# Kernel optimization log

Hardware: AMD Instinct MI355X
Metric: run time of the kernel (lower is better)

The kernel has to match this reference:

```python
import jax, jax.numpy as jnp
import numpy as np

E = 8          # num_experts
TOP_K = 2
D = 512        # embed_dim
H = 1024       # expert_dim = 2 * embed_dim
B, S = 16, 4096


def setup_inputs() -> dict:
    key = jax.random.key(0)
    ks = jax.random.split(key, 10)
    sd = lambda fan_in: 1.0 / np.sqrt(fan_in)
    x = jax.random.normal(ks[0], (B, S, D), dtype=jnp.float32)
    # gate: Linear(D, D//2) -> ReLU -> Linear(D//2, E)
    gw1 = jax.random.uniform(ks[1], (D, D // 2), jnp.float32, -sd(D), sd(D))
    gb1 = jnp.zeros((D // 2,), jnp.float32)
    gw2 = jax.random.uniform(ks[2], (D // 2, E), jnp.float32, -sd(D // 2), sd(D // 2))
    gb2 = jnp.zeros((E,), jnp.float32)
    # stacked experts: Linear(D, H) -> GELU -> Linear(H, D)  (dropout inactive / eval)
    we1 = jax.random.uniform(ks[3], (E, D, H), jnp.float32, -sd(D), sd(D))
    be1 = jnp.zeros((E, H), jnp.float32)
    we2 = jax.random.uniform(ks[4], (E, H, D), jnp.float32, -sd(H), sd(H))
    be2 = jnp.zeros((E, D), jnp.float32)
    return {"x": x, "gw1": gw1, "gb1": gb1, "gw2": gw2, "gb2": gb2,
            "we1": we1, "be1": be1, "we2": we2, "be2": be2}


def reference(x, gw1, gb1, gw2, gb2, we1, be1, we2, be2):
    b, s, d = x.shape
    xf = x.reshape(-1, d)                              # [T, D]
    T = xf.shape[0]

    # Gating network: softmax over experts
    gate_logits = jax.nn.relu(xf @ gw1 + gb1) @ gw2 + gb2   # [T, E]
    gate_weights = jax.nn.softmax(gate_logits, axis=-1)

    # Top-k selection, then re-softmax over the selected probabilities
    # (matches torch: softmax applied to the top-k *probabilities*)
    top_w, top_idx = jax.lax.top_k(gate_weights, TOP_K)    # [T, K]
    top_w = jax.nn.softmax(top_w, axis=-1)

    # Combine weights per (token, expert): zero where expert not selected
    combine = jnp.zeros((T, E), dtype=xf.dtype)
    combine = combine.at[jnp.arange(T)[:, None], top_idx].add(top_w)  # [T, E]

    # Expert MLPs (dropout in eval mode is identity); weight-by-combine is
    # mathematically identical to the masked dispatch in the original.
    out = jnp.zeros_like(xf)
    for e in range(E):
        h = jax.nn.gelu(xf @ we1[e] + be1[e], approximate=False)  # [T, H]
        y = h @ we2[e] + be2[e]                                   # [T, D]
        out = out + combine[:, e:e + 1] * y

    return out.reshape(b, s, d)
```

## Files before the change

### kernel.cpp

```cpp
#include <hip/hip_runtime.h>
#include <hip/hip_bf16.h>
#include <math.h>


typedef __attribute__((ext_vector_type(8))) short bf16x8;
typedef __attribute__((ext_vector_type(4))) float f32x4;

__device__ __forceinline__ unsigned short f2bf(float f){
  unsigned u = __builtin_bit_cast(unsigned, f);
  u += 0x7FFFu + ((u >> 16) & 1u);
  return (unsigned short)(u >> 16);
}

__device__ __forceinline__ bf16x8 cvt8(float4 f0, float4 f1){
  bf16x8 r;
  r[0]=(short)f2bf(f0.x); r[1]=(short)f2bf(f0.y); r[2]=(short)f2bf(f0.z); r[3]=(short)f2bf(f0.w);
  r[4]=(short)f2bf(f1.x); r[5]=(short)f2bf(f1.y); r[6]=(short)f2bf(f1.z); r[7]=(short)f2bf(f1.w);
  return r;
}

__device__ __forceinline__ void gload16(const void* g, void* l){
  __builtin_amdgcn_global_load_lds((const __attribute__((address_space(1))) unsigned int*)g,
                                   (__attribute__((address_space(3))) unsigned int*)l, 16, 0, 0);
}

__global__ __launch_bounds__(256)
void xcvt_kernel(const float* __restrict__ x, unsigned short* __restrict__ xbf){
  int i = blockIdx.x * 256 + threadIdx.x;
  const float4 f0 = ((const float4*)x)[(size_t)i * 2];
  const float4 f1 = ((const float4*)x)[(size_t)i * 2 + 1];
  ushort4 o0, o1;
  o0.x = f2bf(f0.x); o0.y = f2bf(f0.y); o0.z = f2bf(f0.z); o0.w = f2bf(f0.w);
  o1.x = f2bf(f1.x); o1.y = f2bf(f1.y); o1.z = f2bf(f1.z); o1.w = f2bf(f1.w);
  ((ushort4*)xbf)[(size_t)i * 2]     = o0;
  ((ushort4*)xbf)[(size_t)i * 2 + 1] = o1;
}

__global__ __launch_bounds__(256, 4)
void transpose_cvt_kernel(const float* __restrict__ in, unsigned short* __restrict__ out,
                          int R, int C){
  const int tilesR = R >> 6, tilesC = C >> 6;
  const int b = blockIdx.x;
  const int e = b / (tilesR * tilesC);
  const int rem = b % (tilesR * tilesC);
  const int rb = (rem / tilesC) << 6;
  const int cb = (rem % tilesC) << 6;
  const float* src = in + (size_t)e * R * C;
  unsigned short* dst = out + (size_t)e * R * C;
  __shared__ float t[64][65];
  const int r0 = threadIdx.x >> 4;
  const int c4 = (threadIdx.x & 15) << 2;
  #pragma unroll
  for (int p = 0; p < 4; ++p){
    int r = r0 + (p << 4);
    const float4 v = *(const float4*)(src + (size_t)(rb + r) * C + cb + c4);
    t[r][c4+0] = v.x; t[r][c4+1] = v.y; t[r][c4+2] = v.z; t[r][c4+3] = v.w;
  }
  __syncthreads();
  #pragma unroll
  for (int p = 0; p < 4; ++p){
    int cr = r0 + (p << 4);
    ushort4 o;
    o.x = f2bf(t[c4+0][cr]); o.y = f2bf(t[c4+1][cr]);
    o.z = f2bf(t[c4+2][cr]); o.w = f2bf(t[c4+3][cr]);
    *(ushort4*)(dst + (size_t)(cb + cr) * R + rb + c4) = o;
  }
}

__global__ __launch_bounds__(512, 4)
void gate_gemm1_kernel(const float* __restrict__ x, const float* __restrict__ gw1,
                       const float* __restrict__ gb1, float* __restrict__ h){
  __shared__ float xs[32][68];
  __shared__ float g1s[32][256];
  const int tid = threadIdx.x;
  const int t0 = blockIdx.x << 6;
  const int tg = tid >> 6;
  const int cg = tid & 63;

  const int xtok = tid >> 3, xk4 = (tid & 7) << 2;
  const int gr = tid >> 6, gc = (tid & 63) << 2;

  float acc0[4] = {0.f,0.f,0.f,0.f}, acc1[4] = {0.f,0.f,0.f,0.f};
  float acc2[4] = {0.f,0.f,0.f,0.f}, acc3[4] = {0.f,0.f,0.f,0.f};
  float acc4[4] = {0.f,0.f,0.f,0.f}, acc5[4] = {0.f,0.f,0.f,0.f};
  float acc6[4] = {0.f,0.f,0.f,0.f}, acc7[4] = {0.f,0.f,0.f,0.f};

  for (int kb = 0; kb < 512; kb += 32){
    __syncthreads();
    {
      const float4 v = *(const float4*)(x + (size_t)(t0 + xtok) * 512 + kb + xk4);
      xs[xk4+0][xtok] = v.x; xs[xk4+1][xtok] = v.y;
      xs[xk4+2][xtok] = v.z; xs[xk4+3][xtok] = v.w;
    }
    #pragma unroll
    for (int p = 0; p < 4; ++p)
      *(float4*)&g1s[(p << 3) + gr][gc] =
        *(const float4*)(gw1 + (size_t)(kb + (p << 3) + gr) * 256 + gc);
    __syncthreads();
    #pragma unroll 4
    for (int k = 0; k < 32; ++k){
      const float4 wv = *(const float4*)&g1s[k][cg << 2];
      const float4 xa = *(const float4*)&xs[k][tg << 3];
      const float4 xb = *(const float4*)&xs[k][(tg << 3) + 4];
      acc0[0]=fmaf(xa.x,wv.x,acc0[0]); acc0[1]=fmaf(xa.x,wv.y,acc0[1]);
      acc0[2]=fmaf(xa.x,wv.z,acc0[2]); acc0[3]=fmaf(xa.x,wv.w,acc0[3]);
      acc1[0]=fmaf(xa.y,wv.x,acc1[0]); acc1[1]=fmaf(xa.y,wv.y,acc1[1]);
      acc1[2]=fmaf(xa.y,wv.z,acc1[2]); acc1[3]=fmaf(xa.y,wv.w,acc1[3]);
      acc2[0]=fmaf(xa.z,wv.x,acc2[0]); acc2[1]=fmaf(xa.z,wv.y,acc2[1]);
      acc2[2]=fmaf(xa.z,wv.z,acc2[2]); acc2[3]=fmaf(xa.z,wv.w,acc2[3]);
      acc3[0]=fmaf(xa.w,wv.x,acc3[0]); acc3[1]=fmaf(xa.w,wv.y,acc3[1]);
      acc3[2]=fmaf(xa.w,wv.z,acc3[2]); acc3[3]=fmaf(xa.w,wv.w,acc3[3]);
      acc4[0]=fmaf(xb.x,wv.x,acc4[0]); acc4[1]=fmaf(xb.x,wv.y,acc4[1]);
      acc4[2]=fmaf(xb.x,wv.z,acc4[2]); acc4[3]=fmaf(xb.x,wv.w,acc4[3]);
      acc5[0]=fmaf(xb.y,wv.x,acc5[0]); acc5[1]=fmaf(xb.y,wv.y,acc5[1]);
      acc5[2]=fmaf(xb.y,wv.z,acc5[2]); acc5[3]=fmaf(xb.y,wv.w,acc5[3]);
      acc6[0]=fmaf(xb.z,wv.x,acc6[0]); acc6[1]=fmaf(xb.z,wv.y,acc6[1]);
      acc6[2]=fmaf(xb.z,wv.z,acc6[2]); acc6[3]=fmaf(xb.z,wv.w,acc6[3]);
      acc7[0]=fmaf(xb.w,wv.x,acc7[0]); acc7[1]=fmaf(xb.w,wv.y,acc7[1]);
      acc7[2]=fmaf(xb.w,wv.z,acc7[2]); acc7[3]=fmaf(xb.w,wv.w,acc7[3]);
    }
  }

  const float4 bias = *(const float4*)(gb1 + (cg << 2));
  float* hp = h + (size_t)(t0 + (tg << 3)) * 256 + (cg << 2);
  float4 o;
  #define HOUT(ACC, T) \
    o.x = fmaxf(ACC[0] + bias.x, 0.f); o.y = fmaxf(ACC[1] + bias.y, 0.f); \
    o.z = fmaxf(ACC[2] + bias.z, 0.f); o.w = fmaxf(ACC[3] + bias.w, 0.f); \
    *(float4*)(hp + (size_t)(T) * 256) = o;
  HOUT(acc0, 0) HOUT(acc1, 1) HOUT(acc2, 2) HOUT(acc3, 3)
  HOUT(acc4, 4) HOUT(acc5, 5) HOUT(acc6, 6) HOUT(acc7, 7)
  #undef HOUT
}

__global__ __launch_bounds__(256, 2)
void gate2_kernel(const float* __restrict__ h, const float* __restrict__ gw2,
                  const float* __restrict__ gb2,
                  int* __restrict__ counts, int* __restrict__ pair_tok,
                  float* __restrict__ pair_w){
  __shared__ float g2s[256 * 9];
  __shared__ int   lcnt[8];
  __shared__ int   lbase[8];
  __shared__ int   lpre[9];
  __shared__ int   ltok[8][256];
  __shared__ float lw[8][256];
  const int tid = threadIdx.x;
  const int t0 = blockIdx.x << 8;

  #pragma unroll
  for (int p = 0; p < 8; ++p){
    int idx = tid + (p << 8);
    g2s[(idx >> 3) * 9 + (idx & 7)] = gw2[idx];
  }
  if (tid < 8) lcnt[tid] = 0;
  __syncthreads();

  const int token = t0 + tid;
  float pl[8];
  #pragma unroll
  for (int e = 0; e < 8; ++e) pl[e] = gb2[e];
  for (int j = 0; j < 64; ++j){
    const float4 hv = *(const float4*)(h + (size_t)token * 256 + (j << 2));
    #pragma unroll
    for (int i = 0; i < 4; ++i){
      const float hx = ((const float*)&hv)[i];
      #pragma unroll
      for (int e = 0; e < 8; ++e)
        pl[e] = fmaf(hx, g2s[((j << 2) + i) * 9 + e], pl[e]);
    }
  }
  float m = pl[0];
  #pragma unroll
  for (int e = 1; e < 8; ++e) m = fmaxf(m, pl[e]);
  float p[8]; float s = 0.f;
  #pragma unroll
  for (int e = 0; e < 8; ++e){ p[e] = expf(pl[e] - m); s += p[e]; }
  float inv = 1.f / s;
  float m1 = -1.f, m2 = -1.f; int i1 = 0, i2 = 0;
  #pragma unroll
  for (int e = 0; e < 8; ++e){
    float pe = p[e] * inv;
    if (pe > m1){ m2 = m1; i2 = i1; m1 = pe; i1 = e; }
    else if (pe > m2){ m2 = pe; i2 = e; }
  }
  float e21 = expf(m2 - m1);
  float w1 = 1.f / (1.f + e21);
  float w2 = 1.f - w1;
  int p1 = atomicAdd(&lcnt[i1], 1); ltok[i1][p1] = token; lw[i1][p1] = w1;
  int p2 = atomicAdd(&lcnt[i2], 1); ltok[i2][p2] = token; lw[i2][p2] = w2;
  __syncthreads();
  if (tid < 8) lbase[tid] = atomicAdd(&counts[tid], lcnt[tid]);
  if (tid == 0){
    lpre[0] = 0;
    #pragma unroll
    for (int e = 0; e < 8; ++e) lpre[e+1] = lpre[e] + lcnt[e];
  }
  __syncthreads();
  const int total = lpre[8];
  for (int idx = tid; idx < total; idx += 256){
    int e = 0;
    #pragma unroll
    for (int q = 0; q < 7; ++q) e += (idx >= lpre[q + 1]) ? 1 : 0;
    const int i = idx - lpre[e];
    const int dst = (e << 16) + lbase[e] + i;
    pair_tok[dst] = ltok[e][i];
    pair_w[dst]   = lw[e][i];
  }
}

__global__ void scan_kernel(const int* __restrict__ counts, int* __restrict__ offs,
                            int* __restrict__ toffs){
  if (threadIdx.x == 0){
    int o = 0, t = 0;
    #pragma unroll
    for (int e = 0; e < 8; ++e){
      offs[e] = o; o += (counts[e] + 127) >> 7;
      toffs[e] = t; t += counts[e];
    }
    offs[8] = o; toffs[8] = t;
  }
}

__global__ __launch_bounds__(256, 4)
void eg1_kernel(const unsigned short* __restrict__ xbf,
                const unsigned short* __restrict__ we1T,
                const float* __restrict__ be1,
                const int* __restrict__ counts, const int* __restrict__ offs,
                const int* __restrict__ toffs, const int* __restrict__ pair_tok,
                unsigned short* __restrict__ h){
  const int g = (blockIdx.x & 7) * 1032 + (blockIdx.x >> 3);
  const int chunk = g >> 3, nt = g & 7;
  if (chunk >= offs[8]) return;
  int e = 0;
  #pragma unroll
  for (int q = 0; q < 7; ++q) e += (chunk >= offs[q+1]) ? 1 : 0;
  const int cnt = counts[e];
  const int base = (chunk - offs[e]) << 7;
  const int n0 = nt << 7;
  const int tid = threadIdx.x;
  const int lane = tid & 63;
  const int wv = tid >> 6;
  const int wr = wv >> 1, wc = wv & 1;
  const int lrow = lane & 15, kgrp = lane >> 4;

  __shared__ char lds[32768];
  char* const As = lds;
  char* const Bs = lds + 16384;

  const int srow = tid >> 3;
  const int sdelta = ((tid & 7) << 4) ^ ((srow & 7) << 4);
  unsigned aoff[4];
  #pragma unroll
  for (int i = 0; i < 4; ++i){
    int rr = base + srow + (i << 5);
    int tok = (rr < cnt) ? pair_tok[(e << 16) + rr] : 0;
    aoff[i] = ((unsigned)tok) << 10;
  }
  const char* const xb  = (const char*)xbf;
  const char* const w1b = (const char*)we1T + ((size_t)e << 20);

  f32x4 acc[4][4];
  #pragma unroll
  for (int i = 0; i < 4; ++i)
    #pragma unroll
    for (int j = 0; j < 4; ++j) acc[i][j] = (f32x4)0.f;

  const int sw = (lrow & 7) << 4;
  for (int kb = 0; kb < 8; ++kb){
    #pragma unroll
    for (int i = 0; i < 4; ++i)
      gload16(xb + aoff[i] + (kb << 7) + sdelta, As + (tid << 4) + (i << 12));
    #pragma unroll
    for (int i = 0; i < 4; ++i)
      gload16(w1b + (size_t)(n0 + srow + (i << 5)) * 1024 + (kb << 7) + sdelta,
              Bs + (tid << 4) + (i << 12));
    __syncthreads();
    #pragma unroll
    for (int s = 0; s < 2; ++s){
      const int kbyte = ((s << 6) + (kgrp << 4)) ^ sw;
      bf16x8 af[4], bf[4];
      #pragma unroll
      for (int f = 0; f < 4; ++f){
        af[f] = *(const bf16x8*)(As + ((wr << 6) + (f << 4) + lrow) * 128 + kbyte);
        bf[f] = *(const bf16x8*)(Bs + ((wc << 6) + (f << 4) + lrow) * 128 + kbyte);
      }
      #pragma unroll
      for (int fb = 0; fb < 4; ++fb)
        #pragma unroll
        for (int fa = 0; fa < 4; ++fa)
          acc[fb][fa] = __builtin_amdgcn_mfma_f32_16x16x32_bf16(bf[fb], af[fa], acc[fb][fa], 0, 0, 0);
    }
    __syncthreads();
  }

  const int hrow0 = toffs[e] + base;
  float4 bias4[4];
  #pragma unroll
  for (int fb = 0; fb < 4; ++fb)
    bias4[fb] = *(const float4*)(be1 + (e << 10) + n0 + (wc << 6) + (fb << 4) + (kgrp << 2));
  #pragma unroll
  for (int fa = 0; fa < 4; ++fa){
    const int tl = (wr << 6) + (fa << 4) + lrow;
    if (base + tl < cnt){
      unsigned short* hp = h + (size_t)(hrow0 + tl) * 1024 + n0 + (wc << 6) + (kgrp << 2);
      #pragma unroll
      for (int fb = 0; fb < 4; ++fb){
        float v, gl; ushort4 o;
        v = acc[fb][fa][0] + bias4[fb].x; gl = 0.5f*v*(1.f+erff(v*0.70710678118654752f)); o.x = f2bf(gl);
        v = acc[fb][fa][1] + bias4[fb].y; gl = 0.5f*v*(1.f+erff(v*0.70710678118654752f)); o.y = f2bf(gl);
        v = acc[fb][fa][2] + bias4[fb].z; gl = 0.5f*v*(1.f+erff(v*0.70710678118654752f)); o.z = f2bf(gl);
        v = acc[fb][fa][3] + bias4[fb].w; gl = 0.5f*v*(1.f+erff(v*0.70710678118654752f)); o.w = f2bf(gl);
        *(ushort4*)(hp + (fb << 4)) = o;
      }
    }
  }
}

__global__ __launch_bounds__(256, 4)
void eg2_kernel(const unsigned short* __restrict__ h,
                const unsigned short* __restrict__ we2T,
                const float* __restrict__ be2,
                const int* __restrict__ counts, const int* __restrict__ offs,
                const int* __restrict__ toffs, const int* __restrict__ pair_tok,
                const float* __restrict__ pair_w,
                float* __restrict__ out){
  const int g = (blockIdx.x & 7) * 516 + (blockIdx.x >> 3);
  const int chunk = g >> 2, nt = g & 3;
  if (chunk >= offs[8]) return;
  int e = 0;
  #pragma unroll
  for (int q = 0; q < 7; ++q) e += (chunk >= offs[q+1]) ? 1 : 0;
  const int cnt = counts[e];
  const int base = (chunk - offs[e]) << 7;
  const int n0 = nt << 7;
  const int tid = threadIdx.x;
  const int lane = tid & 63;
  const int wv = tid >> 6;
  const int wr = wv >> 1, wc = wv & 1;
  const int lrow = lane & 15, kgrp = lane >> 4;

  __shared__ char lds[32768];
  char* const As = lds;
  char* const Bs = lds + 16384;

  const int srow = tid >> 3;
  const int sdelta = ((tid & 7) << 4) ^ ((srow & 7) << 4);
  const char* const hb  = (const char*)h + (size_t)(toffs[e] + base) * 2048;
  const char* const w2b = (const char*)we2T + ((size_t)e << 20);

  f32x4 acc[4][4];
  #pragma unroll
  for (int i = 0; i < 4; ++i)
    #pragma unroll
    for (int j = 0; j < 4; ++j) acc[i][j] = (f32x4)0.f;

  const int sw = (lrow & 7) << 4;
  for (int kb = 0; kb < 16; ++kb){
    #pragma unroll
    for (int i = 0; i < 4; ++i)
      gload16(hb + (size_t)(srow + (i << 5)) * 2048 + (kb << 7) + sdelta,
              As + (tid << 4) + (i << 12));
    #pragma unroll
    for (int i = 0; i < 4; ++i)
      gload16(w2b + (size_t)(n0 + srow + (i << 5)) * 2048 + (kb << 7) + sdelta,
              Bs + (tid << 4) + (i << 12));
    __syncthreads();
    #pragma unroll
    for (int s = 0; s < 2; ++s){
      const int kbyte = ((s << 6) + (kgrp << 4)) ^ sw;
      bf16x8 af[4], bf[4];
      #pragma unroll
      for (int f = 0; f < 4; ++f){
        af[f] = *(const bf16x8*)(As + ((wr << 6) + (f << 4) + lrow) * 128 + kbyte);
        bf[f] = *(const bf16x8*)(Bs + ((wc << 6) + (f << 4) + lrow) * 128 + kbyte);
      }
      #pragma unroll
      for (int fr = 0; fr < 4; ++fr)
        #pragma unroll
        for (int fc = 0; fc < 4; ++fc)
          acc[fr][fc] = __builtin_amdgcn_mfma_f32_16x16x32_bf16(af[fr], bf[fc], acc[fr][fc], 0, 0, 0);
    }
    __syncthreads();
  }

  float bias2[4];
  #pragma unroll
  for (int fc = 0; fc < 4; ++fc)
    bias2[fc] = be2[(e << 9) + n0 + (wc << 6) + (fc << 4) + lrow];

  #pragma unroll
  for (int fr = 0; fr < 4; ++fr){
    #pragma unroll
    for (int rg = 0; rg < 4; ++rg){
      const int rloc = (wr << 6) + (fr << 4) + (kgrp << 2) + rg;
      const int r = base + rloc;
      if (r < cnt){
        const int tok = pair_tok[(e << 16) + r];
        const float wgt = pair_w[(e << 16) + r];
        float* const orow = out + (size_t)tok * 512 + n0 + (wc << 6) + lrow;
        #pragma unroll
        for (int fc = 0; fc < 4; ++fc)
          atomicAdd(orow + (fc << 4), wgt * (acc[fr][fc][rg] + bias2[fc]));
      }
    }
  }
}

#define VW2() asm volatile("s_waitcnt vmcnt(2)" ::: "memory")
#define BAR() __builtin_amdgcn_s_barrier()
#define SB0() __builtin_amdgcn_sched_barrier(0)

#define G1_MFMA(S, BUF) do{ \
  __builtin_amdgcn_s_setprio(1); \
  _Pragma("unroll") \
  for (int ct = 0; ct < 4; ++ct){ \
    const int col = (ct << 4) + lrow; \
    const int swc = (col & 7) << 4; \
    _Pragma("unroll") \
    for (int k2 = 0; k2 < 4; ++k2){ \
      const int byt = (col << 8) + ((((k2) << 6) + (kgrp << 4)) ^ swc); \
      bf16x8 bfr = *(const bf16x8*)((const char*)(BUF) + byt); \
      hacc[ct] = __builtin_amdgcn_mfma_f32_16x16x32_bf16(a[(S)*4 + k2], bfr, hacc[ct], 0, 0, 0); \
    } \
  } \
  __builtin_amdgcn_s_setprio(0); \
}while(0)

#define G2_MFMA(NB, BUF) do{ \
  __builtin_amdgcn_s_setprio(1); \
  _Pragma("unroll") \
  for (int nt2 = 0; nt2 < 8; ++nt2){ \
    const int col = (nt2 << 4) + lrow; \
    const int swc = (col & 7) << 4; \
    _Pragma("unroll") \
    for (int k2 = 0; k2 < 2; ++k2){ \
      const int byt = (col << 7) + (((k2 << 6) + (kgrp << 4)) ^ swc); \
      bf16x8 bfr = *(const bf16x8*)((const char*)(BUF) + byt); \
      acc[(NB)*8 + nt2] = __builtin_amdgcn_mfma_f32_16x16x32_bf16(a2[k2], bfr, acc[(NB)*8 + nt2], 0, 0, 0); \
    } \
  } \
  __builtin_amdgcn_s_setprio(0); \
}while(0)

#define PHASE(STAGE_STMT, MFMA_STMT) do{ \
  STAGE_STMT; VW2(); BAR(); SB0(); MFMA_STMT; SB0(); BAR(); }while(0)

__global__ __launch_bounds__(512, 2)
void expert_kernel(const unsigned short* __restrict__ xbf,
                   const unsigned short* __restrict__ we1T,
                   const unsigned short* __restrict__ we2T,
                   const float* __restrict__ be1, const float* __restrict__ be2,
                   const int* __restrict__ counts, const int* __restrict__ offs,
                   const int* __restrict__ pair_tok, const float* __restrict__ pair_w,
                   float* __restrict__ out){
  const int b = blockIdx.x;
  if (b >= offs[8]) return;
  int e = 0;
  #pragma unroll
  for (int q = 0; q < 7; ++q) e += (b >= offs[q + 1]) ? 1 : 0;
  const int cnt = counts[e];
  const int base = (b - offs[e]) << 7;
  const int tid = threadIdx.x;
  const int wv = tid >> 6;
  const int lane = tid & 63;
  const int lrow = lane & 15;
  const int kgrp = lane >> 4;

  __shared__ unsigned short w1s0[64 * 128];
  __shared__ unsigned short w1s1[64 * 128];
  __shared__ unsigned short w2s0[128 * 64];
  __shared__ unsigned short w2s1[128 * 64];
  __shared__ unsigned short hs[128 * 64];

  bf16x8 a[16];
  {
    int r = base + (wv << 4) + lrow;
    int tok = (r < cnt) ? pair_tok[(e << 16) + r] : 0;
    const unsigned short* xr = xbf + (size_t)tok * 512 + (kgrp << 3);
    #pragma unroll
    for (int kc = 0; kc < 16; ++kc)
      a[kc] = *(const bf16x8*)(xr + (kc << 5));
  }
  f32x4 acc[32];
  #pragma unroll
  for (int i = 0; i < 32; ++i) acc[i] = (f32x4)0.f;

  const unsigned short* w1g = we1T + ((size_t)e << 19);
  const unsigned short* w2g = we2T + ((size_t)e << 19);

  auto stage_w1 = [&](int hcv, int s, unsigned short* buf){
    #pragma unroll
    for (int i = 0; i < 2; ++i){
      int bb = (((wv << 1) + i) << 10) + (lane << 4);
      int row = bb >> 8;
      int inner = bb & 255;
      int srcb = ((hcv + row) << 10) + (s << 8) + (inner ^ ((row & 7) << 4));
      gload16((const char*)w1g + srcb, (char*)buf + (((wv << 1) + i) << 10));
    }
  };
  auto stage_w2 = [&](int hcv, int nb, unsigned short* buf){
    #pragma unroll
    for (int i = 0; i < 2; ++i){
      int bb = (((wv << 1) + i) << 10) + (lane << 4);
      int row = bb >> 7;
      int inner = bb & 127;
      int srcb = (((nb << 7) + row) << 11) + (hcv << 1) + (inner ^ ((row & 7) << 4));
      gload16((const char*)w2g + srcb, (char*)buf + (((wv << 1) + i) << 10));
    }
  };

  stage_w1(0, 0, w1s0);

  for (int hc = 0; hc < 1024; hc += 64){
    f32x4 hacc[4];
    #pragma unroll
    for (int i = 0; i < 4; ++i) hacc[i] = (f32x4)0.f;

    PHASE(stage_w1(hc, 1, w1s1), G1_MFMA(0, w1s0));
    PHASE(stage_w1(hc, 2, w1s0), G1_MFMA(1, w1s1));
    PHASE(stage_w1(hc, 3, w1s1), G1_MFMA(2, w1s0));
    PHASE(stage_w2(hc, 0, w2s0), G1_MFMA(3, w1s1));

    bf16x8 a2[2];
    {
      char* const hsb = (char*)hs;
      #pragma unroll
      for (int ct = 0; ct < 4; ++ct){
        int colL = (ct << 4) + lrow;
        float bias = be1[(e << 10) + hc + colL];
        #pragma unroll
        for (int rr = 0; rr < 4; ++rr){
          int rowL = (wv << 4) + (kgrp << 2) + rr;
          float v = hacc[ct][rr] + bias;
          float g = 0.5f * v * (1.f + erff(v * 0.70710678118654752f));
          int byt = (rowL << 7) + (colL << 1);
          *(unsigned short*)(hsb + (byt ^ ((rowL & 7) << 4))) = f2bf(g);
        }
      }
      const char* const hsc = (const char*)hs;
      int rowL = (wv << 4) + lrow;
      int swr = (rowL & 7) << 4;
      #pragma unroll
      for (int k2 = 0; k2 < 2; ++k2){
        int byt = (rowL << 7) + (((k2 << 6) + (kgrp << 4)) ^ swr);
        a2[k2] = *(const bf16x8*)(hsc + byt);
      }
    }

    PHASE(stage_w2(hc, 1, w2s1),               G2_MFMA(0, w2s0));
    PHASE(stage_w2(hc, 2, w2s0),               G2_MFMA(1, w2s1));
    PHASE(stage_w2(hc, 3, w2s1),               G2_MFMA(2, w2s0));
    PHASE(stage_w1((hc + 64) & 1023, 0, w1s0), G2_MFMA(3, w2s1));
  }

  #pragma unroll
  for (int rr = 0; rr < 4; ++rr){
    int rowL = (wv << 4) + (kgrp << 2) + rr;
    int rg = base + rowL;
    if (rg < cnt){
      int tok = pair_tok[(e << 16) + rg];
      float wp = pair_w[(e << 16) + rg];
      float* orow = out + (size_t)tok * 512;
      #pragma unroll
      for (int tl = 0; tl < 32; ++tl){
        int col = (tl << 4) + lrow;
        atomicAdd(orow + col, wp * (acc[tl][rr] + be2[(e << 9) + col]));
      }
    }
  }
}

extern "C" void kernel_launch(void* const* d_in, const int* in_sizes, int n_in,
                              void* d_out, int out_size, void* d_ws, size_t ws_size,
                              hipStream_t stream){
  const float* x   = (const float*)d_in[0];
  const float* gw1 = (const float*)d_in[1];
  const float* gb1 = (const float*)d_in[2];
  const float* gw2 = (const float*)d_in[3];
  const float* gb2 = (const float*)d_in[4];
  const float* we1 = (const float*)d_in[5];
  const float* be1 = (const float*)d_in[6];
  const float* we2 = (const float*)d_in[7];
  const float* be2 = (const float*)d_in[8];
  float* out = (float*)d_out;

  char* ws = (char*)d_ws;
  const size_t MiB = 1024 * 1024;
  unsigned short* we1T = (unsigned short*)(ws);
  unsigned short* we2T = (unsigned short*)(ws + 8 * MiB);
  int*   pair_tok = (int*)  (ws + 16 * MiB);
  float* pair_w   = (float*)(ws + 18 * MiB);
  int*   counts   = (int*)  (ws + 20 * MiB);
  int*   offs     = (int*)  (ws + 20 * MiB + 256);
  int*   toffs    = (int*)  (ws + 20 * MiB + 512);
  unsigned short* xbf  = (unsigned short*)(ws + 21 * MiB);
  float* ghuf          = (float*)(ws + 85 * MiB);
  unsigned short* hexp = (unsigned short*)(ws + 85 * MiB);
  const bool big = ws_size >= 344 * MiB;

  hipMemsetAsync(d_out, 0, (size_t)out_size * sizeof(float), stream);
  hipMemsetAsync(counts, 0, 256, stream);

  hipLaunchKernelGGL(xcvt_kernel, dim3(16384), dim3(256), 0, stream, x, xbf);
  hipLaunchKernelGGL(transpose_cvt_kernel, dim3(1024), dim3(256), 0, stream,
                     we1, we1T, 512, 1024);
  hipLaunchKernelGGL(transpose_cvt_kernel, dim3(1024), dim3(256), 0, stream,
                     we2, we2T, 1024, 512);
  hipLaunchKernelGGL(gate_gemm1_kernel, dim3(1024), dim3(512), 0, stream,
                     x, gw1, gb1, ghuf);
  hipLaunchKernelGGL(gate2_kernel, dim3(256), dim3(256), 0, stream,
                     ghuf, gw2, gb2, counts, pair_tok, pair_w);
  hipLaunchKernelGGL(scan_kernel, dim3(1), dim3(64), 0, stream, counts, offs, toffs);

  if (big){
    hipLaunchKernelGGL(eg1_kernel, dim3(8256), dim3(256), 0, stream,
                       xbf, we1T, be1, counts, offs, toffs, pair_tok, hexp);
    hipLaunchKernelGGL(eg2_kernel, dim3(4128), dim3(256), 0, stream,
                       hexp, we2T, be2, counts, offs, toffs, pair_tok, pair_w, out);
  } else {
    hipLaunchKernelGGL(expert_kernel, dim3(1032), dim3(512), 0, stream,
                       xbf, we1T, we2T, be1, be2, counts, offs, pair_tok, pair_w, out);
  }
}
```

Before: 799.6 us.

## Double-buffer LDS in expert GEMMs, fuse x conversion into gate GEMM, drop fused path

Result: slower. 895.1 us (+11.9%).

```diff
diff --git a/kernel.cpp b/kernel.cpp
--- a/kernel.cpp
+++ b/kernel.cpp
@@ -12,28 +12,9 @@
   return (unsigned short)(u >> 16);
 }
 
-__device__ __forceinline__ bf16x8 cvt8(float4 f0, float4 f1){
-  bf16x8 r;
-  r[0]=(short)f2bf(f0.x); r[1]=(short)f2bf(f0.y); r[2]=(short)f2bf(f0.z); r[3]=(short)f2bf(f0.w);
-  r[4]=(short)f2bf(f1.x); r[5]=(short)f2bf(f1.y); r[6]=(short)f2bf(f1.z); r[7]=(short)f2bf(f1.w);
-  return r;
-}
-
 __device__ __forceinline__ void gload16(const void* g, void* l){
   __builtin_amdgcn_global_load_lds((const __attribute__((address_space(1))) unsigned int*)g,
                                    (__attribute__((address_space(3))) unsigned int*)l, 16, 0, 0);
-}
-
-__global__ __launch_bounds__(256)
-void xcvt_kernel(const float* __restrict__ x, unsigned short* __restrict__ xbf){
-  int i = blockIdx.x * 256 + threadIdx.x;
-  const float4 f0 = ((const float4*)x)[(size_t)i * 2];
-  const float4 f1 = ((const float4*)x)[(size_t)i * 2 + 1];
-  ushort4 o0, o1;
-  o0.x = f2bf(f0.x); o0.y = f2bf(f0.y); o0.z = f2bf(f0.z); o0.w = f2bf(f0.w);
-  o1.x = f2bf(f1.x); o1.y = f2bf(f1.y); o1.z = f2bf(f1.z); o1.w = f2bf(f1.w);
-  ((ushort4*)xbf)[(size_t)i * 2]     = o0;
-  ((ushort4*)xbf)[(size_t)i * 2 + 1] = o1;
 }
 
 __global__ __launch_bounds__(256, 4)
@@ -69,7 +50,8 @@
 
 __global__ __launch_bounds__(512, 4)
 void gate_gemm1_kernel(const float* __restrict__ x, const float* __restrict__ gw1,
-                       const float* __restrict__ gb1, float* __restrict__ h){
+                       const float* __restrict__ gb1, float* __restrict__ h,
+                       unsigned short* __restrict__ xbf){
   __shared__ float xs[32][68];
   __shared__ float g1s[32][256];
   const int tid = threadIdx.x;
@@ -91,6 +73,9 @@
       const float4 v = *(const float4*)(x + (size_t)(t0 + xtok) * 512 + kb + xk4);
       xs[xk4+0][xtok] = v.x; xs[xk4+1][xtok] = v.y;
       xs[xk4+2][xtok] = v.z; xs[xk4+3][xtok] = v.w;
+      ushort4 o;
+      o.x = f2bf(v.x); o.y = f2bf(v.y); o.z = f2bf(v.z); o.w = f2bf(v.w);
+      *(ushort4*)(xbf + (size_t)(t0 + xtok) * 512 + kb + xk4) = o;
     }
     #pragma unroll
     for (int p = 0; p < 4; ++p)
@@ -221,7 +206,7 @@
   }
 }
 
-__global__ __launch_bounds__(256, 4)
+__global__ __launch_bounds__(256, 2)
 void eg1_kernel(const unsigned short* __restrict__ xbf,
                 const unsigned short* __restrict__ we1T,
                 const float* __restrict__ be1,
@@ -243,9 +228,7 @@
   const int wr = wv >> 1, wc = wv & 1;
   const int lrow = lane & 15, kgrp = lane >> 4;
 
-  __shared__ char lds[32768];
-  char* const As = lds;
-  char* const Bs = lds + 16384;
+  __shared__ char lds[65536];
 
   const int srow = tid >> 3;
   const int sdelta = ((tid & 7) << 4) ^ ((srow & 7) << 4);
@@ -265,16 +248,24 @@
     #pragma unroll
     for (int j = 0; j < 4; ++j) acc[i][j] = (f32x4)0.f;
 
-  const int sw = (lrow & 7) << 4;
-  for (int kb = 0; kb < 8; ++kb){
+  auto stage = [&](int kb, char* dbase){
     #pragma unroll
     for (int i = 0; i < 4; ++i)
-      gload16(xb + aoff[i] + (kb << 7) + sdelta, As + (tid << 4) + (i << 12));
+      gload16(xb + aoff[i] + (kb << 7) + sdelta, dbase + (tid << 4) + (i << 12));
     #pragma unroll
     for (int i = 0; i < 4; ++i)
       gload16(w1b + (size_t)(n0 + srow + (i << 5)) * 1024 + (kb << 7) + sdelta,
-              Bs + (tid << 4) + (i << 12));
-    __syncthreads();
+              dbase + 16384 + (tid << 4) + (i << 12));
+  };
+
+  const int sw = (lrow & 7) << 4;
+  stage(0, lds);
+  __syncthreads();
+  int cur = 0;
+  for (int kb = 0; kb < 8; ++kb){
+    if (kb < 7) stage(kb + 1, lds + ((cur ^ 1) << 15));
+    const char* const As = lds + (cur << 15);
+    const char* const Bs = As + 16384;
     #pragma unroll
     for (int s = 0; s < 2; ++s){
       const int kbyte = ((s << 6) + (kgrp << 4)) ^ sw;
@@ -290,7 +281,11 @@
         for (int fa = 0; fa < 4; ++fa)
           acc[fb][fa] = __builtin_amdgcn_mfma_f32_16x16x32_bf16(bf[fb], af[fa], acc[fb][fa], 0, 0, 0);
     }
-    __syncthreads();
+    if (kb < 7){
+      asm volatile("s_waitcnt vmcnt(0)" ::: "memory");
+      __builtin_amdgcn_s_barrier();
+    }
+    cur ^= 1;
   }
 
   const int hrow0 = toffs[e] + base;
@@ -316,7 +311,7 @@
   }
 }
 
-__global__ __launch_bounds__(256, 4)
+__global__ __launch_bounds__(256, 2)
 void eg2_kernel(const unsigned short* __restrict__ h,
                 const unsigned short* __restrict__ we2T,
                 const float* __restrict__ be2,
@@ -339,9 +334,7 @@
   const int wr = wv >> 1, wc = wv & 1;
   const int lrow = lane & 15, kgrp = lane >> 4;
 
-  __shared__ char lds[32768];
-  char* const As = lds;
-  char* const Bs = lds + 16384;
+  __shared__ char lds[65536];
 
   const int srow = tid >> 3;
   const int sdelta = ((tid & 7) << 4) ^ ((srow & 7) << 4);
@@ -354,17 +347,25 @@
     #pragma unroll
     for (int j = 0; j < 4; ++j) acc[i][j] = (f32x4)0.f;
 
-  const int sw = (lrow & 7) << 4;
-  for (int kb = 0; kb < 16; ++kb){
+  auto stage = [&](int kb, char* dbase){
     #pragma unroll
     for (int i = 0; i < 4; ++i)
       gload16(hb + (size_t)(srow + (i << 5)) * 2048 + (kb << 7) + sdelta,
-              As + (tid << 4) + (i << 12));
+              dbase + (tid << 4) + (i << 12));
     #pragma unroll
     for (int i = 0; i < 4; ++i)
       gload16(w2b + (size_t)(n0 + srow + (i << 5)) * 2048 + (kb << 7) + sdelta,
-              Bs + (tid << 4) + (i << 12));
-    __syncthreads();
+              dbase + 16384 + (tid << 4) + (i << 12));
+  };
+
+  const int sw = (lrow & 7) << 4;
+  stage(0, lds);
+  __syncthreads();
+  int cur = 0;
+  for (int kb = 0; kb < 16; ++kb){
+    if (kb < 15) stage(kb + 1, lds + ((cur ^ 1) << 15));
+    const char* const As = lds + (cur << 15);
+    const char* const Bs = As + 16384;
     #pragma unroll
     for (int s = 0; s < 2; ++s){
       const int kbyte = ((s << 6) + (kgrp << 4)) ^ sw;
@@ -380,7 +381,11 @@
         for (int fc = 0; fc < 4; ++fc)
           acc[fr][fc] = __builtin_amdgcn_mfma_f32_16x16x32_bf16(af[fr], bf[fc], acc[fr][fc], 0, 0, 0);
     }
-    __syncthreads();
+    if (kb < 15){
+      asm volatile("s_waitcnt vmcnt(0)" ::: "memory");
+      __builtin_amdgcn_s_barrier();
+    }
+    cur ^= 1;
   }
 
   float bias2[4];
@@ -401,170 +406,6 @@
         #pragma unroll
         for (int fc = 0; fc < 4; ++fc)
           atomicAdd(orow + (fc << 4), wgt * (acc[fr][fc][rg] + bias2[fc]));
-      }
-    }
-  }
-}
-
-#define VW2() asm volatile("s_waitcnt vmcnt(2)" ::: "memory")
-#define BAR() __builtin_amdgcn_s_barrier()
-#define SB0() __builtin_amdgcn_sched_barrier(0)
-
-#define G1_MFMA(S, BUF) do{ \
-  __builtin_amdgcn_s_setprio(1); \
-  _Pragma("unroll") \
-  for (int ct = 0; ct < 4; ++ct){ \
-    const int col = (ct << 4) + lrow; \
-    const int swc = (col & 7) << 4; \
-    _Pragma("unroll") \
-    for (int k2 = 0; k2 < 4; ++k2){ \
-      const int byt = (col << 8) + ((((k2) << 6) + (kgrp << 4)) ^ swc); \
-      bf16x8 bfr = *(const bf16x8*)((const char*)(BUF) + byt); \
-      hacc[ct] = __builtin_amdgcn_mfma_f32_16x16x32_bf16(a[(S)*4 + k2], bfr, hacc[ct], 0, 0, 0); \
-    } \
-  } \
-  __builtin_amdgcn_s_setprio(0); \
-}while(0)
-
-#define G2_MFMA(NB, BUF) do{ \
-  __builtin_amdgcn_s_setprio(1); \
-  _Pragma("unroll") \
-  for (int nt2 = 0; nt2 < 8; ++nt2){ \
-    const int col = (nt2 << 4) + lrow; \
-    const int swc = (col & 7) << 4; \
-    _Pragma("unroll") \
-    for (int k2 = 0; k2 < 2; ++k2){ \
-      const int byt = (col << 7) + (((k2 << 6) + (kgrp << 4)) ^ swc); \
-      bf16x8 bfr = *(const bf16x8*)((const char*)(BUF) + byt); \
-      acc[(NB)*8 + nt2] = __builtin_amdgcn_mfma_f32_16x16x32_bf16(a2[k2], bfr, acc[(NB)*8 + nt2], 0, 0, 0); \
-    } \
-  } \
-  __builtin_amdgcn_s_setprio(0); \
-}while(0)
-
-#define PHASE(STAGE_STMT, MFMA_STMT) do{ \
-  STAGE_STMT; VW2(); BAR(); SB0(); MFMA_STMT; SB0(); BAR(); }while(0)
-
-__global__ __launch_bounds__(512, 2)
-void expert_kernel(const unsigned short* __restrict__ xbf,
-                   const unsigned short* __restrict__ we1T,
-                   const unsigned short* __restrict__ we2T,
-                   const float* __restrict__ be1, const float* __restrict__ be2,
-                   const int* __restrict__ counts, const int* __restrict__ offs,
-                   const int* __restrict__ pair_tok, const float* __restrict__ pair_w,
-                   float* __restrict__ out){
-  const int b = blockIdx.x;
-  if (b >= offs[8]) return;
-  int e = 0;
-  #pragma unroll
-  for (int q = 0; q < 7; ++q) e += (b >= offs[q + 1]) ? 1 : 0;
-  const int cnt = counts[e];
-  const int base = (b - offs[e]) << 7;
-  const int tid = threadIdx.x;
-  const int wv = tid >> 6;
-  const int lane = tid & 63;
-  const int lrow = lane & 15;
-  const int kgrp = lane >> 4;
-
-  __shared__ unsigned short w1s0[64 * 128];
-  __shared__ unsigned short w1s1[64 * 128];
-  __shared__ unsigned short w2s0[128 * 64];
-  __shared__ unsigned short w2s1[128 * 64];
-  __shared__ unsigned short hs[128 * 64];
-
-  bf16x8 a[16];
-  {
-    int r = base + (wv << 4) + lrow;
-    int tok = (r < cnt) ? pair_tok[(e << 16) + r] : 0;
-    const unsigned short* xr = xbf + (size_t)tok * 512 + (kgrp << 3);
-    #pragma unroll
-    for (int kc = 0; kc < 16; ++kc)
-      a[kc] = *(const bf16x8*)(xr + (kc << 5));
-  }
-  f32x4 acc[32];
-  #pragma unroll
-  for (int i = 0; i < 32; ++i) acc[i] = (f32x4)0.f;
-
-  const unsigned short* w1g = we1T + ((size_t)e << 19);
-  const unsigned short* w2g = we2T + ((size_t)e << 19);
-
-  auto stage_w1 = [&](int hcv, int s, unsigned short* buf){
-    #pragma unroll
-    for (int i = 0; i < 2; ++i){
-      int bb = (((wv << 1) + i) << 10) + (lane << 4);
-      int row = bb >> 8;
-      int inner = bb & 255;
-      int srcb = ((hcv + row) << 10) + (s << 8) + (inner ^ ((row & 7) << 4));
-      gload16((const char*)w1g + srcb, (char*)buf + (((wv << 1) + i) << 10));
-    }
-  };
-  auto stage_w2 = [&](int hcv, int nb, unsigned short* buf){
-    #pragma unroll
-    for (int i = 0; i < 2; ++i){
-      int bb = (((wv << 1) + i) << 10) + (lane << 4);
-      int row = bb >> 7;
-      int inner = bb & 127;
-      int srcb = (((nb << 7) + row) << 11) + (hcv << 1) + (inner ^ ((row & 7) << 4));
-      gload16((const char*)w2g + srcb, (char*)buf + (((wv << 1) + i) << 10));
-    }
-  };
-
-  stage_w1(0, 0, w1s0);
-
-  for (int hc = 0; hc < 1024; hc += 64){
-    f32x4 hacc[4];
-    #pragma unroll
-    for (int i = 0; i < 4; ++i) hacc[i] = (f32x4)0.f;
-
-    PHASE(stage_w1(hc, 1, w1s1), G1_MFMA(0, w1s0));
-    PHASE(stage_w1(hc, 2, w1s0), G1_MFMA(1, w1s1));
-    PHASE(stage_w1(hc, 3, w1s1), G1_MFMA(2, w1s0));
-    PHASE(stage_w2(hc, 0, w2s0), G1_MFMA(3, w1s1));
-
-    bf16x8 a2[2];
-    {
-      char* const hsb = (char*)hs;
-      #pragma unroll
-      for (int ct = 0; ct < 4; ++ct){
-        int colL = (ct << 4) + lrow;
-        float bias = be1[(e << 10) + hc + colL];
-        #pragma unroll
-        for (int rr = 0; rr < 4; ++rr){
-          int rowL = (wv << 4) + (kgrp << 2) + rr;
-          float v = hacc[ct][rr] + bias;
-          float g = 0.5f * v * (1.f + erff(v * 0.70710678118654752f));
-          int byt = (rowL << 7) + (colL << 1);
-          *(unsigned short*)(hsb + (byt ^ ((rowL & 7) << 4))) = f2bf(g);
-        }
-      }
-      const char* const hsc = (const char*)hs;
-      int rowL = (wv << 4) + lrow;
-      int swr = (rowL & 7) << 4;
-      #pragma unroll
-      for (int k2 = 0; k2 < 2; ++k2){
-        int byt = (rowL << 7) + (((k2 << 6) + (kgrp << 4)) ^ swr);
-        a2[k2] = *(const bf16x8*)(hsc + byt);
-      }
-    }
-
-    PHASE(stage_w2(hc, 1, w2s1),               G2_MFMA(0, w2s0));
-    PHASE(stage_w2(hc, 2, w2s0),               G2_MFMA(1, w2s1));
-    PHASE(stage_w2(hc, 3, w2s1),               G2_MFMA(2, w2s0));
-    PHASE(stage_w1((hc + 64) & 1023, 0, w1s0), G2_MFMA(3, w2s1));
-  }
-
-  #pragma unroll
-  for (int rr = 0; rr < 4; ++rr){
-    int rowL = (wv << 4) + (kgrp << 2) + rr;
-    int rg = base + rowL;
-    if (rg < cnt){
-      int tok = pair_tok[(e << 16) + rg];
-      float wp = pair_w[(e << 16) + rg];
-      float* orow = out + (size_t)tok * 512;
-      #pragma unroll
-      for (int tl = 0; tl < 32; ++tl){
-        int col = (tl << 4) + lrow;
-        atomicAdd(orow + col, wp * (acc[tl][rr] + be2[(e << 9) + col]));
       }
     }
   }
@@ -596,29 +437,22 @@
   unsigned short* xbf  = (unsigned short*)(ws + 21 * MiB);
   float* ghuf          = (float*)(ws + 85 * MiB);
   unsigned short* hexp = (unsigned short*)(ws + 85 * MiB);
-  const bool big = ws_size >= 344 * MiB;
 
   hipMemsetAsync(d_out, 0, (size_t)out_size * sizeof(float), stream);
   hipMemsetAsync(counts, 0, 256, stream);
 
-  hipLaunchKernelGGL(xcvt_kernel, dim3(16384), dim3(256), 0, stream, x, xbf);
   hipLaunchKernelGGL(transpose_cvt_kernel, dim3(1024), dim3(256), 0, stream,
                      we1, we1T, 512, 1024);
   hipLaunchKernelGGL(transpose_cvt_kernel, dim3(1024), dim3(256), 0, stream,
                      we2, we2T, 1024, 512);
   hipLaunchKernelGGL(gate_gemm1_kernel, dim3(1024), dim3(512), 0, stream,
-                     x, gw1, gb1, ghuf);
+                     x, gw1, gb1, ghuf, xbf);
   hipLaunchKernelGGL(gate2_kernel, dim3(256), dim3(256), 0, stream,
                      ghuf, gw2, gb2, counts, pair_tok, pair_w);
   hipLaunchKernelGGL(scan_kernel, dim3(1), dim3(64), 0, stream, counts, offs, toffs);
 
-  if (big){
-    hipLaunchKernelGGL(eg1_kernel, dim3(8256), dim3(256), 0, stream,
-                       xbf, we1T, be1, counts, offs, toffs, pair_tok, hexp);
-    hipLaunchKernelGGL(eg2_kernel, dim3(4128), dim3(256), 0, stream,
-                       hexp, we2T, be2, counts, offs, toffs, pair_tok, pair_w, out);
-  } else {
-    hipLaunchKernelGGL(expert_kernel, dim3(1032), dim3(512), 0, stream,
-                       xbf, we1T, we2T, be1, be2, counts, offs, pair_tok, pair_w, out);
-  }
-}
+  hipLaunchKernelGGL(eg1_kernel, dim3(8256), dim3(256), 0, stream,
+                     xbf, we1T, be1, counts, offs, toffs, pair_tok, hexp);
+  hipLaunchKernelGGL(eg2_kernel, dim3(4128), dim3(256), 0, stream,
+                     hexp, we2T, be2, counts, offs, toffs, pair_tok, pair_w, out);
+}
```
